# Kernel tuning notes

Hardware: AMD Instinct MI355X
Metric: run time of the kernel (lower is better)

## Reference

```python
import jax, jax.numpy as jnp
import numpy as np

N_NODES = 100000
N_REL = 3
N_EDGES = 400000
D = 128


def setup_inputs() -> dict:
    key = jax.random.key(0)
    k_x, k_e, k_w = jax.random.split(key, 3)
    x = jax.random.normal(k_x, (N_NODES, D), dtype=jnp.float32)
    edges = jax.random.randint(k_e, (N_REL, 2, N_EDGES), 0, N_NODES, dtype=jnp.int64)
    # GraphConv weight per relation (glorot-ish scale) and bias
    W = jax.random.normal(k_w, (N_REL, D, D), dtype=jnp.float32) / np.sqrt(D)
    b = jnp.zeros((N_REL, D), dtype=jnp.float32)
    return {"x": x, "edges": edges, "W": W, "b": b}


def reference(x, edges, W, b):
    """HetGraphLayer with GCN convs per edge type, mean channel-combine.

    Each relation: dgl GraphConv with norm='both':
      out = D_in^{-1/2} * A^T * (D_out^{-1/2} * x @ W) + b
    with degrees clamped to min 1 (allow_zero_in_degree=True).
    """
    N = x.shape[0]

    def per_rel(e, Wr, br):
        src, dst = e[0], e[1]  # [E]
        ones = jnp.ones(src.shape, dtype=x.dtype)
        deg_out = jnp.maximum(jax.ops.segment_sum(ones, src, num_segments=N), 1.0)
        deg_in = jnp.maximum(jax.ops.segment_sum(ones, dst, num_segments=N), 1.0)
        h = (x * jax.lax.rsqrt(deg_out)[:, None]) @ Wr          # [N, D]
        agg = jax.ops.segment_sum(h[src], dst, num_segments=N)  # [N, D]
        return agg * jax.lax.rsqrt(deg_in)[:, None] + br

    rel_embs = jax.vmap(per_rel)(edges, W, b)  # [R, N, D] (torch.stack over etypes)
    return jnp.mean(rel_embs, axis=0)          # ChannelCombine 'mean'
```

## Files before the change

kernel.cpp:

```cpp
#include <hip/hip_runtime.h>
#include <hip/hip_fp16.h>
#include <math.h>

#define N_NODES 100000
#define N_RELS  3
#define N_EDGES 400000
#define D       128
#define NTOT    (N_RELS * N_NODES)
#define ELL_W   12
#define OVF_CAP 4096
#define CPAD    3
#define GEMM_BLKS 782
#define FILL_CHUNKS 391
#define FILL_BLKS (FILL_CHUNKS * 3)

typedef _Float16 f16x8 __attribute__((ext_vector_type(8)));
typedef float    f32x4 __attribute__((ext_vector_type(4)));

__global__ void prep_w_kernel(const float* __restrict__ W, const float* __restrict__ b,
                              ushort* __restrict__ Wt, float* __restrict__ bsum) {
    int id = blockIdx.x * 256 + threadIdx.x;
    if (id < 3 * D * D) {
        int r = id >> 14;
        int rem = id & 16383;
        int k = rem >> 7, j = rem & 127;
        Wt[r * 16384 + j * 128 + k] = __builtin_bit_cast(ushort, (_Float16)W[id]);
    }
    if (blockIdx.x == 0 && threadIdx.x < D) {
        int j = threadIdx.x;
        bsum[j] = (b[j] + b[D + j] + b[2 * D + j]) * (1.0f / 3.0f);
    }
}

__global__ __launch_bounds__(256) void fused_kernel(
    const float* __restrict__ x, const ushort* __restrict__ Wt,
    const int* __restrict__ edges, ushort* __restrict__ h,
    int* __restrict__ deg_pad, int* __restrict__ cur_pad,
    int* __restrict__ ell, int* __restrict__ ovf_cnt, int2* __restrict__ ovf) {
    const int bid = blockIdx.x;
    const int tid = threadIdx.x;
    const bool is_gemm = (bid < 2 * GEMM_BLKS) && ((bid & 1) == 0);

    if (is_gemm) {
        __shared__ ushort Bt[128 * 128];
        const int n0 = (bid >> 1) * 128;
        const int w = tid >> 6, l = tid & 63;
        const int wrow = w * 32;
        const int lr = l & 15, lk = (l >> 4) * 8;

        f16x8 a[2][4];
        #pragma unroll
        for (int fi = 0; fi < 2; ++fi) {
            int row = n0 + wrow + fi * 16 + lr;
            row = min(row, N_NODES - 1);
            const float* xp = x + (size_t)row * 128 + lk;
            #pragma unroll
            for (int ks = 0; ks < 4; ++ks) {
                float4 va = *(const float4*)(xp + ks * 32);
                float4 vb = *(const float4*)(xp + ks * 32 + 4);
                f16x8 t;
                t[0] = (_Float16)va.x; t[1] = (_Float16)va.y;
                t[2] = (_Float16)va.z; t[3] = (_Float16)va.w;
                t[4] = (_Float16)vb.x; t[5] = (_Float16)vb.y;
                t[6] = (_Float16)vb.z; t[7] = (_Float16)vb.w;
                a[fi][ks] = t;
            }
        }

        for (int rel = 0; rel < 3; ++rel) {
            __syncthreads();
            {
                const ushort* Wg = Wt + rel * 16384;
                #pragma unroll
                for (int c = 0; c < 8; ++c) {
                    int id = c * 256 + tid;
                    int j = id >> 4, k8 = id & 15;
                    uint4 v = *(const uint4*)(Wg + j * 128 + k8 * 8);
                    int ba = (j * 256 + k8 * 16) ^ ((j & 7) << 4);
                    *(uint4*)((char*)Bt + ba) = v;
                }
            }
            __syncthreads();

            f32x4 acc[2][8];
            #pragma unroll
            for (int fi = 0; fi < 2; ++fi)
                #pragma unroll
                for (int fj = 0; fj < 8; ++fj)
                    acc[fi][fj] = (f32x4){0.f, 0.f, 0.f, 0.f};

            #pragma unroll
            for (int ks = 0; ks < 4; ++ks) {
                f16x8 bfr[8];
                #pragma unroll
                for (int fj = 0; fj < 8; ++fj) {
                    int j = fj * 16 + lr;
                    int ba = (j * 256 + (ks * 32 + lk) * 2) ^ ((j & 7) << 4);
                    bfr[fj] = *(f16x8*)((char*)Bt + ba);
                }
                #pragma unroll
                for (int fi = 0; fi < 2; ++fi)
                    #pragma unroll
                    for (int fj = 0; fj < 8; ++fj)
                        acc[fi][fj] = __builtin_amdgcn_mfma_f32_16x16x32_f16(
                            a[fi][ks], bfr[fj], acc[fi][fj], 0, 0, 0);
            }

            const int cr4 = (l >> 4) * 4;
            #pragma unroll
            for (int fi = 0; fi < 2; ++fi) {
                int rbase = n0 + wrow + fi * 16 + cr4;
                #pragma unroll
                for (int fj = 0; fj < 8; ++fj) {
                    int col = fj * 16 + lr;
                    #pragma unroll
                    for (int i = 0; i < 4; ++i) {
                        int row = rbase + i;
                        if (row < N_NODES)
                            h[(size_t)row * 384 + rel * 128 + col] =
                                __builtin_bit_cast(ushort, (_Float16)acc[fi][fj][i]);
                    }
                }
            }
        }
    } else {
        int fid = (bid < 2 * GEMM_BLKS) ? (bid >> 1) : (bid - GEMM_BLKS);
        int rel = fid / FILL_CHUNKS;
        int chunk = fid - rel * FILL_CHUNKS;
        int e0 = (chunk * 256 + tid) * 4;
        if (e0 >= N_EDGES) return;
        const int* src = edges + (size_t)(rel * 2 + 0) * N_EDGES;
        const int* dst = edges + (size_t)(rel * 2 + 1) * N_EDGES;
        int4 s4 = *(const int4*)(src + e0);
        int4 t4 = *(const int4*)(dst + e0);
        int ss[4] = {s4.x, s4.y, s4.z, s4.w};
        int tt[4] = {t4.x, t4.y, t4.z, t4.w};
        #pragma unroll
        for (int k = 0; k < 4; ++k) {
            atomicAdd(deg_pad + ((size_t)(rel * N_NODES + ss[k]) << CPAD), 1);
            int p = atomicAdd(cur_pad + ((size_t)(rel * N_NODES + tt[k]) << CPAD), 1);
            if (p < ELL_W) {
                ell[(size_t)(rel * N_NODES + tt[k]) * ELL_W + p] = ss[k];
            } else {
                int i = atomicAdd(ovf_cnt, 1);
                if (i < OVF_CAP) ovf[i] = make_int2(ss[k], tt[k] | (rel << 20));
            }
        }
    }
}

__global__ __launch_bounds__(256) void gather_kernel(
    const ushort* __restrict__ h, const int* __restrict__ deg_pad,
    const int* __restrict__ cur_pad, const int* __restrict__ ell,
    const float* __restrict__ bsum, float* __restrict__ out) {
    int w = threadIdx.x >> 6, l = threadIdx.x & 63;
    int n = blockIdx.x * 4 + w;
    if (n >= N_NODES) return;
    float ox = 0.f, oy = 0.f;
    #pragma unroll
    for (int r = 0; r < 3; ++r) {
        int base = r * N_NODES + n;
        int deg = cur_pad[(size_t)base << CPAD];
        int cnt = min(deg, ELL_W);
        int e = 0;
        float sc = 0.f;
        if (l < cnt) {
            e = ell[(size_t)base * ELL_W + l];
            sc = rsqrtf((float)max(deg_pad[(size_t)(r * N_NODES + e) << CPAD], 1));
        }
        float ax = 0.f, ay = 0.f;
        int i = 0;
        for (; i + 2 <= cnt; i += 2) {
            int s0 = __shfl(e, i), s1 = __shfl(e, i + 1);
            float c0 = __shfl(sc, i), c1 = __shfl(sc, i + 1);
            uint u0 = *(const uint*)(h + (size_t)s0 * 384 + r * 128 + 2 * l);
            uint u1 = *(const uint*)(h + (size_t)s1 * 384 + r * 128 + 2 * l);
            __half2 h0 = __builtin_bit_cast(__half2, u0);
            __half2 h1 = __builtin_bit_cast(__half2, u1);
            ax = fmaf(__low2float(h0), c0, ax);
            ay = fmaf(__high2float(h0), c0, ay);
            ax = fmaf(__low2float(h1), c1, ax);
            ay = fmaf(__high2float(h1), c1, ay);
        }
        if (i < cnt) {
            int s0 = __shfl(e, i);
            float c0 = __shfl(sc, i);
            uint u0 = *(const uint*)(h + (size_t)s0 * 384 + r * 128 + 2 * l);
            __half2 h0 = __builtin_bit_cast(__half2, u0);
            ax = fmaf(__low2float(h0), c0, ax);
            ay = fmaf(__high2float(h0), c0, ay);
        }
        float rdi = rsqrtf((float)max(deg, 1));
        ox = fmaf(ax, rdi, ox);
        oy = fmaf(ay, rdi, oy);
    }
    float2 bs = *(const float2*)(bsum + 2 * l);
    float2 o;
    o.x = ox * (1.f / 3.f) + bs.x;
    o.y = oy * (1.f / 3.f) + bs.y;
    *(float2*)(out + (size_t)n * 128 + 2 * l) = o;
}

__global__ void ovf_kernel(const ushort* __restrict__ h, const int* __restrict__ deg_pad,
                           const int* __restrict__ cur_pad,
                           const int* __restrict__ ovf_cnt, const int2* __restrict__ ovf,
                           float* out) {
    int m = min(*ovf_cnt, OVF_CAP);
    int total = m * 64;
    for (int idx = blockIdx.x * blockDim.x + threadIdx.x; idx < total;
         idx += blockDim.x * gridDim.x) {
        int ent = idx >> 6, l = idx & 63;
        int s = ovf[ent].x;
        int packed = ovf[ent].y;
        int t = packed & 0xFFFFF, r = packed >> 20;
        uint u = *(const uint*)(h + (size_t)s * 384 + r * 128 + 2 * l);
        __half2 hv = __builtin_bit_cast(__half2, u);
        float rdo = rsqrtf((float)max(deg_pad[(size_t)(r * N_NODES + s) << CPAD], 1));
        float rdi = rsqrtf((float)max(cur_pad[(size_t)(r * N_NODES + t) << CPAD], 1));
        float sc = rdo * rdi * (1.f / 3.f);
        atomicAdd(out + (size_t)t * 128 + 2 * l + 0, __low2float(hv) * sc);
        atomicAdd(out + (size_t)t * 128 + 2 * l + 1, __high2float(hv) * sc);
    }
}

extern "C" void kernel_launch(void* const* d_in, const int* in_sizes, int n_in,
                              void* d_out, int out_size, void* d_ws, size_t ws_size,
                              hipStream_t stream) {
    const float* x     = (const float*)d_in[0];
    const int*   edges = (const int*)d_in[1];
    const float* W     = (const float*)d_in[2];
    const float* b     = (const float*)d_in[3];
    float* out = (float*)d_out;

    char* ws = (char*)d_ws;
    size_t off = 0;
    auto alloc = [&](size_t bytes) -> void* {
        void* p = ws + off;
        off += (bytes + 255) & ~(size_t)255;
        return p;
    };
    int*   deg_pad = (int*)alloc(((size_t)NTOT << CPAD) * 4);
    int*   cur_pad = (int*)alloc(((size_t)NTOT << CPAD) * 4);
    int*   ovf_cnt = (int*)alloc(256);
    size_t zero_bytes = off;
    float* bsum    = (float*)alloc((size_t)D * 4);
    ushort* Wt     = (ushort*)alloc((size_t)3 * D * D * 2);
    int2*  ovf     = (int2*)alloc((size_t)OVF_CAP * 8);
    int*   ell     = (int*)alloc((size_t)NTOT * ELL_W * 4);
    ushort* h      = (ushort*)alloc((size_t)N_NODES * 3 * D * 2);

    hipMemsetAsync(ws, 0, zero_bytes, stream);
    prep_w_kernel<<<192, 256, 0, stream>>>(W, b, Wt, bsum);
    fused_kernel<<<GEMM_BLKS + FILL_BLKS, 256, 0, stream>>>(
        x, Wt, edges, h, deg_pad, cur_pad, ell, ovf_cnt, ovf);
    gather_kernel<<<(N_NODES + 3) / 4, 256, 0, stream>>>(
        h, deg_pad, cur_pad, ell, bsum, out);
    ovf_kernel<<<16, 256, 0, stream>>>(h, deg_pad, cur_pad, ovf_cnt, ovf, out);
}
```

Measured before the change: 210.6 us.

## Replace global atomic ELL build with two-pass bucketed partition via LDS

Edge processing no longer uses a global atomic per edge on padded degree and cursor arrays. A first pass, run inside the fused GEMM kernel, builds per-chunk histograms in LDS and scatters edges into 512-node buckets. A new second kernel then builds the ELL rows and in- and out-degrees per bucket with LDS atomics and writes them out coalesced. This removes scattered global atomics and the 8x-padded counters, which also shrinks the memset, at the cost of an extra kernel launch and a partition buffer with a fixed capacity (BCAP) that silently drops edges if a bucket overflows.

Measured after the change: 174.5 us. -17.1%, faster.

```diff
diff --git a/kernel.cpp b/kernel.cpp
--- a/kernel.cpp
+++ b/kernel.cpp
@@ -9,10 +9,13 @@
 #define NTOT    (N_RELS * N_NODES)
 #define ELL_W   12
 #define OVF_CAP 4096
-#define CPAD    3
-#define GEMM_BLKS 782
-#define FILL_CHUNKS 391
-#define FILL_BLKS (FILL_CHUNKS * 3)
+#define BSH     9
+#define NB      196
+#define BCAP    3072
+#define CHUNK   4096
+#define NCH     98
+#define PASS1_BLKS (NCH * N_RELS)
+#define GEMM_BLKS  782
 
 typedef _Float16 f16x8 __attribute__((ext_vector_type(8)));
 typedef float    f32x4 __attribute__((ext_vector_type(4)));
@@ -35,15 +38,23 @@
 __global__ __launch_bounds__(256) void fused_kernel(
     const float* __restrict__ x, const ushort* __restrict__ Wt,
     const int* __restrict__ edges, ushort* __restrict__ h,
-    int* __restrict__ deg_pad, int* __restrict__ cur_pad,
-    int* __restrict__ ell, int* __restrict__ ovf_cnt, int2* __restrict__ ovf) {
+    int2* __restrict__ part_dst, int* __restrict__ part_src,
+    int* __restrict__ gcur_dst, int* __restrict__ gcur_src) {
+    __shared__ union {
+        ushort Bt[128 * 128];
+        struct { int s[CHUNK]; int t[CHUNK]; } st;
+    } U;
+    __shared__ int histd[NB], hists[NB], segd[NB], segs[NB];
+
     const int bid = blockIdx.x;
     const int tid = threadIdx.x;
-    const bool is_gemm = (bid < 2 * GEMM_BLKS) && ((bid & 1) == 0);
-
-    if (is_gemm) {
-        __shared__ ushort Bt[128 * 128];
-        const int n0 = (bid >> 1) * 128;
+    bool is_fill;
+    int gid;
+    if (bid < 2 * PASS1_BLKS) { is_fill = (bid & 1); gid = bid >> 1; }
+    else                      { is_fill = false;     gid = bid - PASS1_BLKS; }
+
+    if (!is_fill) {
+        const int n0 = gid * 128;
         const int w = tid >> 6, l = tid & 63;
         const int wrow = w * 32;
         const int lr = l & 15, lk = (l >> 4) * 8;
@@ -77,7 +88,7 @@
                     int j = id >> 4, k8 = id & 15;
                     uint4 v = *(const uint4*)(Wg + j * 128 + k8 * 8);
                     int ba = (j * 256 + k8 * 16) ^ ((j & 7) << 4);
-                    *(uint4*)((char*)Bt + ba) = v;
+                    *(uint4*)((char*)U.Bt + ba) = v;
                 }
             }
             __syncthreads();
@@ -96,7 +107,7 @@
                 for (int fj = 0; fj < 8; ++fj) {
                     int j = fj * 16 + lr;
                     int ba = (j * 256 + (ks * 32 + lk) * 2) ^ ((j & 7) << 4);
-                    bfr[fj] = *(f16x8*)((char*)Bt + ba);
+                    bfr[fj] = *(f16x8*)((char*)U.Bt + ba);
                 }
                 #pragma unroll
                 for (int fi = 0; fi < 2; ++fi)
@@ -124,34 +135,87 @@
             }
         }
     } else {
-        int fid = (bid < 2 * GEMM_BLKS) ? (bid >> 1) : (bid - GEMM_BLKS);
-        int rel = fid / FILL_CHUNKS;
-        int chunk = fid - rel * FILL_CHUNKS;
-        int e0 = (chunk * 256 + tid) * 4;
-        if (e0 >= N_EDGES) return;
+        const int rel   = gid / NCH;
+        const int chunk = gid - rel * NCH;
+        const int e0 = chunk * CHUNK;
+        const int ne = min(CHUNK, N_EDGES - e0);
         const int* src = edges + (size_t)(rel * 2 + 0) * N_EDGES;
         const int* dst = edges + (size_t)(rel * 2 + 1) * N_EDGES;
-        int4 s4 = *(const int4*)(src + e0);
-        int4 t4 = *(const int4*)(dst + e0);
-        int ss[4] = {s4.x, s4.y, s4.z, s4.w};
-        int tt[4] = {t4.x, t4.y, t4.z, t4.w};
-        #pragma unroll
-        for (int k = 0; k < 4; ++k) {
-            atomicAdd(deg_pad + ((size_t)(rel * N_NODES + ss[k]) << CPAD), 1);
-            int p = atomicAdd(cur_pad + ((size_t)(rel * N_NODES + tt[k]) << CPAD), 1);
-            if (p < ELL_W) {
-                ell[(size_t)(rel * N_NODES + tt[k]) * ELL_W + p] = ss[k];
-            } else {
-                int i = atomicAdd(ovf_cnt, 1);
-                if (i < OVF_CAP) ovf[i] = make_int2(ss[k], tt[k] | (rel << 20));
-            }
-        }
-    }
+
+        for (int i = tid; i < NB; i += 256) { histd[i] = 0; hists[i] = 0; }
+        __syncthreads();
+        for (int i = tid; i < ne; i += 256) {
+            int s = src[e0 + i], t = dst[e0 + i];
+            U.st.s[i] = s; U.st.t[i] = t;
+            atomicAdd(&histd[t >> BSH], 1);
+            atomicAdd(&hists[s >> BSH], 1);
+        }
+        __syncthreads();
+        for (int i = tid; i < NB; i += 256) {
+            int hd = histd[i];
+            segd[i] = hd ? atomicAdd(&gcur_dst[rel * NB + i], hd) : 0;
+            int hs = hists[i];
+            segs[i] = hs ? atomicAdd(&gcur_src[rel * NB + i], hs) : 0;
+            histd[i] = 0; hists[i] = 0;
+        }
+        __syncthreads();
+        for (int i = tid; i < ne; i += 256) {
+            int s = U.st.s[i], t = U.st.t[i];
+            int bd = t >> BSH;
+            int p = segd[bd] + atomicAdd(&histd[bd], 1);
+            if (p < BCAP) part_dst[(size_t)(rel * NB + bd) * BCAP + p] = make_int2(s, t);
+            int bs = s >> BSH;
+            int q = segs[bs] + atomicAdd(&hists[bs], 1);
+            if (q < BCAP) part_src[(size_t)(rel * NB + bs) * BCAP + q] = s;
+        }
+    }
+}
+
+__global__ __launch_bounds__(256) void pass2_kernel(
+    const int2* __restrict__ part_dst, const int* __restrict__ part_src,
+    const int* __restrict__ gcur_dst, const int* __restrict__ gcur_src,
+    int* __restrict__ ell, int* __restrict__ deg_in, int* __restrict__ deg_out,
+    int* __restrict__ ovf_cnt, int2* __restrict__ ovf) {
+    __shared__ int cnt[512];
+    __shared__ int lell[512 * ELL_W];
+    const int b = blockIdx.x, rel = blockIdx.y;
+    const int tid = threadIdx.x;
+    const int n0 = b << BSH;
+    const int nvalid = min(512, N_NODES - n0);
+
+    for (int i = tid; i < 512; i += 256) cnt[i] = 0;
+    __syncthreads();
+    const int m = min(gcur_dst[rel * NB + b], BCAP);
+    const int2* pp = part_dst + (size_t)(rel * NB + b) * BCAP;
+    for (int i = tid; i < m; i += 256) {
+        int2 e = pp[i];
+        int li = e.y - n0;
+        int p = atomicAdd(&cnt[li], 1);
+        if (p < ELL_W) lell[li * ELL_W + p] = e.x;
+        else {
+            int o = atomicAdd(ovf_cnt, 1);
+            if (o < OVF_CAP) ovf[o] = make_int2(e.x, e.y | (rel << 20));
+        }
+    }
+    __syncthreads();
+    for (int i = tid; i < nvalid; i += 256)
+        deg_in[rel * N_NODES + n0 + i] = cnt[i];
+    for (int i = tid; i < nvalid * ELL_W; i += 256)
+        ell[(size_t)(rel * N_NODES + n0) * ELL_W + i] = lell[i];
+    __syncthreads();
+    for (int i = tid; i < 512; i += 256) cnt[i] = 0;
+    __syncthreads();
+    const int m2 = min(gcur_src[rel * NB + b], BCAP);
+    const int* ps = part_src + (size_t)(rel * NB + b) * BCAP;
+    for (int i = tid; i < m2; i += 256) atomicAdd(&cnt[ps[i] - n0], 1);
+    __syncthreads();
+    for (int i = tid; i < nvalid; i += 256)
+        deg_out[rel * N_NODES + n0 + i] = cnt[i];
 }
 
 __global__ __launch_bounds__(256) void gather_kernel(
-    const ushort* __restrict__ h, const int* __restrict__ deg_pad,
-    const int* __restrict__ cur_pad, const int* __restrict__ ell,
+    const ushort* __restrict__ h, const int* __restrict__ deg_in,
+    const int* __restrict__ deg_out, const int* __restrict__ ell,
     const float* __restrict__ bsum, float* __restrict__ out) {
     int w = threadIdx.x >> 6, l = threadIdx.x & 63;
     int n = blockIdx.x * 4 + w;
@@ -160,13 +224,13 @@
     #pragma unroll
     for (int r = 0; r < 3; ++r) {
         int base = r * N_NODES + n;
-        int deg = cur_pad[(size_t)base << CPAD];
+        int deg = deg_in[base];
         int cnt = min(deg, ELL_W);
         int e = 0;
         float sc = 0.f;
         if (l < cnt) {
             e = ell[(size_t)base * ELL_W + l];
-            sc = rsqrtf((float)max(deg_pad[(size_t)(r * N_NODES + e) << CPAD], 1));
+            sc = rsqrtf((float)max(deg_out[r * N_NODES + e], 1));
         }
         float ax = 0.f, ay = 0.f;
         int i = 0;
@@ -201,8 +265,8 @@
     *(float2*)(out + (size_t)n * 128 + 2 * l) = o;
 }
 
-__global__ void ovf_kernel(const ushort* __restrict__ h, const int* __restrict__ deg_pad,
-                           const int* __restrict__ cur_pad,
+__global__ void ovf_kernel(const ushort* __restrict__ h, const int* __restrict__ deg_in,
+                           const int* __restrict__ deg_out,
                            const int* __restrict__ ovf_cnt, const int2* __restrict__ ovf,
                            float* out) {
     int m = min(*ovf_cnt, OVF_CAP);
@@ -215,8 +279,8 @@
         int t = packed & 0xFFFFF, r = packed >> 20;
         uint u = *(const uint*)(h + (size_t)s * 384 + r * 128 + 2 * l);
         __half2 hv = __builtin_bit_cast(__half2, u);
-        float rdo = rsqrtf((float)max(deg_pad[(size_t)(r * N_NODES + s) << CPAD], 1));
-        float rdi = rsqrtf((float)max(cur_pad[(size_t)(r * N_NODES + t) << CPAD], 1));
+        float rdo = rsqrtf((float)max(deg_out[r * N_NODES + s], 1));
+        float rdi = rsqrtf((float)max(deg_in[r * N_NODES + t], 1));
         float sc = rdo * rdi * (1.f / 3.f);
         atomicAdd(out + (size_t)t * 128 + 2 * l + 0, __low2float(hv) * sc);
         atomicAdd(out + (size_t)t * 128 + 2 * l + 1, __high2float(hv) * sc);
@@ -239,21 +303,27 @@
         off += (bytes + 255) & ~(size_t)255;
         return p;
     };
-    int*   deg_pad = (int*)alloc(((size_t)NTOT << CPAD) * 4);
-    int*   cur_pad = (int*)alloc(((size_t)NTOT << CPAD) * 4);
-    int*   ovf_cnt = (int*)alloc(256);
+    int*   gcur_dst = (int*)alloc((size_t)N_RELS * NB * 4);
+    int*   gcur_src = (int*)alloc((size_t)N_RELS * NB * 4);
+    int*   ovf_cnt  = (int*)alloc(256);
     size_t zero_bytes = off;
-    float* bsum    = (float*)alloc((size_t)D * 4);
-    ushort* Wt     = (ushort*)alloc((size_t)3 * D * D * 2);
-    int2*  ovf     = (int2*)alloc((size_t)OVF_CAP * 8);
-    int*   ell     = (int*)alloc((size_t)NTOT * ELL_W * 4);
-    ushort* h      = (ushort*)alloc((size_t)N_NODES * 3 * D * 2);
+    float* bsum     = (float*)alloc((size_t)D * 4);
+    ushort* Wt      = (ushort*)alloc((size_t)3 * D * D * 2);
+    int2*  ovf      = (int2*)alloc((size_t)OVF_CAP * 8);
+    int2*  part_dst = (int2*)alloc((size_t)N_RELS * NB * BCAP * 8);
+    int*   part_src = (int*)alloc((size_t)N_RELS * NB * BCAP * 4);
+    int*   ell      = (int*)alloc((size_t)NTOT * ELL_W * 4);
+    int*   deg_in   = (int*)alloc((size_t)NTOT * 4);
+    int*   deg_out  = (int*)alloc((size_t)NTOT * 4);
+    ushort* h       = (ushort*)alloc((size_t)N_NODES * 3 * D * 2);
 
     hipMemsetAsync(ws, 0, zero_bytes, stream);
     prep_w_kernel<<<192, 256, 0, stream>>>(W, b, Wt, bsum);
-    fused_kernel<<<GEMM_BLKS + FILL_BLKS, 256, 0, stream>>>(
-        x, Wt, edges, h, deg_pad, cur_pad, ell, ovf_cnt, ovf);
+    fused_kernel<<<GEMM_BLKS + PASS1_BLKS, 256, 0, stream>>>(
+        x, Wt, edges, h, part_dst, part_src, gcur_dst, gcur_src);
+    pass2_kernel<<<dim3(NB, 3), 256, 0, stream>>>(
+        part_dst, part_src, gcur_dst, gcur_src, ell, deg_in, deg_out, ovf_cnt, ovf);
     gather_kernel<<<(N_NODES + 3) / 4, 256, 0, stream>>>(
-        h, deg_pad, cur_pad, ell, bsum, out);
-    ovf_kernel<<<16, 256, 0, stream>>>(h, deg_pad, cur_pad, ovf_cnt, ovf, out);
-}
+        h, deg_in, deg_out, ell, bsum, out);
+    ovf_kernel<<<16, 256, 0, stream>>>(h, deg_in, deg_out, ovf_cnt, ovf, out);
+}
```
